# Kernel tuning notes

Hardware: AMD Instinct MI355X
Metric: run time of the kernel (lower is better)

The kernel has to match this reference:

```python
import jax, jax.numpy as jnp
import numpy as np

B, C, L = 8, 256, 2048


def setup_inputs() -> dict:
    key = jax.random.key(0)
    ks = jax.random.split(key, 7)
    s = 0.05
    return {
        "x": jax.random.normal(ks[0], (B, C, L), dtype=jnp.float32),
        "Wq": jax.random.normal(ks[1], (C, C), dtype=jnp.float32) * s,
        "bq": jax.random.normal(ks[2], (C,), dtype=jnp.float32) * s,
        "Wk": jax.random.normal(ks[3], (C, C), dtype=jnp.float32) * s,
        "bk": jax.random.normal(ks[4], (C,), dtype=jnp.float32) * s,
        "Wv": jax.random.normal(ks[5], (C, C), dtype=jnp.float32) * s,
        "bv": jax.random.normal(ks[6], (C,), dtype=jnp.float32) * s,
    }


def reference(x, Wq, bq, Wk, bk, Wv, bv):
    # Conv1d with kernel_size=1 == per-position linear over channels.
    # x: [B, C, L]
    scale = x.shape[1] ** (-0.5)
    q = jnp.einsum('oc,bcl->bol', Wq, x) + bq[None, :, None]  # [B,C,L]
    k = jnp.einsum('oc,bcl->bol', Wk, x) + bk[None, :, None]
    v = jnp.einsum('oc,bcl->bol', Wv, x) + bv[None, :, None]
    scores = jnp.einsum('bcl,bcm->blm', q, k) * scale          # [B,L,L]
    attn = jax.nn.softmax(scores, axis=-1)
    context = jnp.einsum('blm,bcm->bcl', attn, v)              # [B,C,L]
    return context + x
```

## Files before the change

### kernel.cpp

```cpp
#include <hip/hip_runtime.h>

#define NB 8
#define NC 256
#define NL 2048
#define SCALE 0.0625f

typedef __attribute__((ext_vector_type(8))) __bf16 bf16x8;
typedef __attribute__((ext_vector_type(4))) float f32x4;
typedef __attribute__((ext_vector_type(4))) unsigned int u32x4;
typedef __attribute__((ext_vector_type(2))) unsigned int u32x2;
typedef __attribute__((ext_vector_type(4))) unsigned short u16x4;
typedef __attribute__((ext_vector_type(8))) unsigned short u16x8;

static __device__ __forceinline__ unsigned short f2b(float f) {
    unsigned int u = __builtin_bit_cast(unsigned int, f);
    u += 0x7fffu + ((u >> 16) & 1u);
    return (unsigned short)(u >> 16);
}

__global__ void wconv_kernel(const float* __restrict__ Wq,
                             const float* __restrict__ Wk,
                             const float* __restrict__ Wv,
                             unsigned short* __restrict__ Wbf)
{
    const int base = (blockIdx.x * 256 + threadIdx.x) * 4;
    const int mat  = base >> 16;
    const int off  = base & 65535;
    const float* W = (mat == 0) ? Wq : (mat == 1) ? Wk : Wv;
    float4 w = *(const float4*)&W[off];
    u16x4 p = {f2b(w.x), f2b(w.y), f2b(w.z), f2b(w.w)};
    *(u16x4*)&Wbf[base] = p;
}

__global__ __launch_bounds__(256, 2) void xprep_kernel(
    const float* __restrict__ x, unsigned short* __restrict__ xT)
{
    const int b  = blockIdx.z;
    const int c0 = blockIdx.y * 64;
    const int l0 = blockIdx.x * 64;
    const int t  = threadIdx.x;

    __shared__ unsigned short Tr[64][68];

    #pragma unroll
    for (int p = 0; p < 4; ++p) {
        const int c  = p * 16 + (t >> 4);
        const int lg = t & 15;
        float4 xv = *(const float4*)&x[((size_t)(b * NC + c0 + c)) * NL + l0 + lg * 4];
        u16x4 pk = {f2b(xv.x), f2b(xv.y), f2b(xv.z), f2b(xv.w)};
        *(u16x4*)&Tr[c][lg * 4] = pk;
    }
    __syncthreads();
    #pragma unroll
    for (int j = 0; j < 2; ++j) {
        const int chunk = t + 256 * j;
        const int l  = chunk >> 3;
        const int ck = chunk & 7;
        u16x8 o;
        #pragma unroll
        for (int i = 0; i < 8; ++i) o[i] = Tr[ck * 8 + i][l];
        *(u16x8*)&xT[((size_t)(b * NL + l0 + l)) * NC + c0 + ck * 8] = o;
    }
}

__global__ __launch_bounds__(256, 2) void qkv_mfma(
    const unsigned short* __restrict__ xT,
    const unsigned short* __restrict__ Wbf,
    const float* __restrict__ bq, const float* __restrict__ bk,
    const float* __restrict__ bv,
    unsigned short* __restrict__ qT, unsigned short* __restrict__ kT,
    unsigned short* __restrict__ vo)
{
    const int raw = blockIdx.x;
    const int b   = raw & 7;
    const int rem = raw >> 3;
    const int mat = rem >> 5;
    const int lt0 = (rem & 31) * 64;
    const int t    = threadIdx.x;
    const int w    = t >> 6;
    const int lane = t & 63;
    const int ln15 = lane & 15;
    const int quad = lane >> 4;

    __shared__ __align__(16) unsigned short XT[64 * 256];
    __shared__ __align__(16) unsigned short WC[256 * 64];

    const unsigned short* Wm = Wbf + mat * 65536;
    const float* bias = (mat == 0) ? bq : (mat == 1) ? bk : bv;

    float bvals[4][4];
    #pragma unroll
    for (int ot = 0; ot < 4; ++ot)
        #pragma unroll
        for (int r = 0; r < 4; ++r)
            bvals[ot][r] = bias[w * 64 + ot * 16 + quad * 4 + r];

    #pragma unroll
    for (int s = 0; s < 8; ++s) {
        const int il = w * 8 + s;
        const int n  = il * 2 + (lane >> 5);
        const int p  = lane & 31;
        const int g  = p ^ (n & 15);
        const unsigned short* gp = &xT[((size_t)(b * NL + lt0 + n)) * NC + g * 8];
        __builtin_amdgcn_global_load_lds(
            (const __attribute__((address_space(1))) unsigned int*)gp,
            (__attribute__((address_space(3))) unsigned int*)&XT[il * 512],
            16, 0, 0);
    }

    f32x4 acc[4][4];
    #pragma unroll
    for (int i = 0; i < 4; ++i)
        #pragma unroll
        for (int j = 0; j < 4; ++j) acc[i][j] = f32x4{0.f, 0.f, 0.f, 0.f};

    for (int k0 = 0; k0 < 4; ++k0) {
        if (k0) __syncthreads();
        #pragma unroll
        for (int s = 0; s < 8; ++s) {
            const int il = w * 8 + s;
            const int o  = il * 8 + (lane >> 3);
            const int p  = lane & 7;
            const int g  = p ^ (o & 7);
            const unsigned short* gp = &Wm[(size_t)o * NC + k0 * 64 + g * 8];
            __builtin_amdgcn_global_load_lds(
                (const __attribute__((address_space(1))) unsigned int*)gp,
                (__attribute__((address_space(3))) unsigned int*)&WC[il * 512],
                16, 0, 0);
        }
        __syncthreads();

        #pragma unroll
        for (int ks = 0; ks < 2; ++ks) {
            bf16x8 xf[4];
            #pragma unroll
            for (int lt = 0; lt < 4; ++lt) {
                const int l  = lt * 16 + ln15;
                const int kc = k0 * 8 + ks * 4 + quad;
                const int pp = kc ^ (l & 15);
                xf[lt] = __builtin_bit_cast(bf16x8, *(const u32x4*)&XT[l * 256 + pp * 8]);
            }
            #pragma unroll
            for (int ot = 0; ot < 4; ++ot) {
                const int o  = w * 64 + ot * 16 + ln15;
                const int pp = (ks * 4 + quad) ^ (o & 7);
                bf16x8 wf = __builtin_bit_cast(bf16x8, *(const u32x4*)&WC[o * 64 + pp * 8]);
                #pragma unroll
                for (int lt = 0; lt < 4; ++lt)
                    acc[ot][lt] = __builtin_amdgcn_mfma_f32_16x16x32_bf16(
                                      wf, xf[lt], acc[ot][lt], 0, 0, 0);
            }
        }
    }

    if (mat < 2) {
        unsigned short* out = (mat == 0) ? qT : kT;
        #pragma unroll
        for (int ot = 0; ot < 4; ++ot) {
            const int o_base = w * 64 + ot * 16 + quad * 4;
            #pragma unroll
            for (int lt = 0; lt < 4; ++lt) {
                const int l = lt0 + lt * 16 + ln15;
                u16x4 pk;
                #pragma unroll
                for (int r = 0; r < 4; ++r)
                    pk[r] = f2b(acc[ot][lt][r] + bvals[ot][r]);
                *(u16x4*)&out[((size_t)(b * NL + l)) * NC + o_base] = pk;
            }
        }
    } else {
        #pragma unroll
        for (int ot = 0; ot < 4; ++ot)
            #pragma unroll
            for (int lt = 0; lt < 4; ++lt) {
                const int l = lt0 + lt * 16 + ln15;
                #pragma unroll
                for (int r = 0; r < 4; ++r) {
                    const int o = w * 64 + ot * 16 + quad * 4 + r;
                    vo[((size_t)(b * NC + o)) * NL + l] = f2b(acc[ot][lt][r] + bvals[ot][r]);
                }
            }
    }
}

__global__ __launch_bounds__(1024, 4) void attn_kernel(
    const unsigned short* __restrict__ qT,
    const unsigned short* __restrict__ kT,
    const unsigned short* __restrict__ v,
    const float* __restrict__ x,
    float* __restrict__ out)
{
    const int raw  = blockIdx.x;
    const int b    = raw & 7;
    const int l0   = (raw >> 3) * 64;
    const int t    = threadIdx.x;
    const int w    = t >> 6;
    const int lane = t & 63;
    const int ln15 = lane & 15;
    const int quad = lane >> 4;
    const int qg   = w & 3;
    const int kg   = w >> 2;

    __shared__ __align__(16) char smem[147456];
    unsigned short* Kb0 = (unsigned short*)smem;
    unsigned short* Vb0 = (unsigned short*)(smem + 32768);
    unsigned short* Kb1 = (unsigned short*)(smem + 65536);
    unsigned short* Vb1 = (unsigned short*)(smem + 98304);
    char* P0 = smem + 131072;
    char* P1 = smem + 139264;
    float (*buf)[68] = (float(*)[68])smem;

    bf16x8 qf[8];
    {
        const size_t qrow = ((size_t)b * NL + l0 + qg * 16 + ln15) * NC;
        #pragma unroll
        for (int kt = 0; kt < 8; ++kt)
            qf[kt] = __builtin_bit_cast(bf16x8,
                        *(const u32x4*)&qT[qrow + kt * 32 + quad * 8]);
    }

    f32x4 ctx[4];
    #pragma unroll
    for (int i = 0; i < 4; ++i) ctx[i] = f32x4{0.f, 0.f, 0.f, 0.f};
    f32x4 dacc = f32x4{0.f, 0.f, 0.f, 0.f};

    const u16x8 ones_u = {0x3F80, 0x3F80, 0x3F80, 0x3F80,
                          0x3F80, 0x3F80, 0x3F80, 0x3F80};
    const bf16x8 onesf = __builtin_bit_cast(bf16x8, ones_u);

    auto stageK = [&](int mt, unsigned short* Kd) {
        const int m0 = mt * 64;
        #pragma unroll
        for (int s = 0; s < 2; ++s) {
            const int il = w * 2 + s;
            const int n  = il * 2 + (lane >> 5);
            const int g  = (lane & 31) ^ (n & 15);
            const unsigned short* gp = &kT[((size_t)b * NL + m0 + n) * NC + g * 8];
            __builtin_amdgcn_global_load_lds(
                (const __attribute__((address_space(1))) unsigned int*)gp,
                (__attribute__((address_space(3))) unsigned int*)&Kd[il * 512],
                16, 0, 0);
        }
    };
    auto stageV = [&](int mt, unsigned short* Vd) {
        const int m0 = mt * 64;
        #pragma unroll
        for (int s = 0; s < 2; ++s) {
            const int il = w * 2 + s;
            const int c  = il * 8 + (lane >> 3);
            const int g  = (lane & 7) ^ (c & 7);
            const unsigned short* gp = &v[((size_t)(b * NC + c)) * NL + m0 + g * 8];
            __builtin_amdgcn_global_load_lds(
                (const __attribute__((address_space(1))) unsigned int*)gp,
                (__attribute__((address_space(3))) unsigned int*)&Vd[il * 512],
                16, 0, 0);
        }
    };

    const int q    = qg * 16 + ln15;
    const int pwof = q * 128 + (((kg * 32) + quad * 8) ^ ((q & 7) << 4));
    int prof[2];
    #pragma unroll
    for (int jw = 0; jw < 2; ++jw)
        prof[jw] = q * 128 + ((jw * 64 + quad * 16) ^ ((q & 7) << 4));

    stageK(0, Kb0);
    __syncthreads();

    for (int mt = 0; mt <= 32; ++mt) {
        if (mt < 31) stageK(mt + 1, (mt & 1) ? Kb0 : Kb1);
        if (mt < 32) stageV(mt, (mt & 1) ? Vb1 : Vb0);

        f32x4 sacc0 = f32x4{0.f, 0.f, 0.f, 0.f};
        f32x4 sacc1 = f32x4{0.f, 0.f, 0.f, 0.f};
        if (mt < 32) {
            const unsigned short* Kd = (mt & 1) ? Kb1 : Kb0;
            const int n = kg * 16 + ln15;
            #pragma unroll
            for (int kt = 0; kt < 8; kt += 2) {
                const int p0 = (kt * 4 + quad) ^ (n & 15);
                const int p1 = ((kt + 1) * 4 + quad) ^ (n & 15);
                bf16x8 kf0 = __builtin_bit_cast(bf16x8,
                               *(const u32x4*)&Kd[n * 256 + p0 * 8]);
                bf16x8 kf1 = __builtin_bit_cast(bf16x8,
                               *(const u32x4*)&Kd[n * 256 + p1 * 8]);
                sacc0 = __builtin_amdgcn_mfma_f32_16x16x32_bf16(
                            kf0, qf[kt], sacc0, 0, 0, 0);
                sacc1 = __builtin_amdgcn_mfma_f32_16x16x32_bf16(
                            kf1, qf[kt + 1], sacc1, 0, 0, 0);
            }
        }

        if (mt > 0) {
            const char* Pr = ((mt - 1) & 1) ? P1 : P0;
            const unsigned short* Vd = ((mt - 1) & 1) ? Vb1 : Vb0;
            bf16x8 pa[2];
            #pragma unroll
            for (int jw = 0; jw < 2; ++jw)
                pa[jw] = __builtin_bit_cast(bf16x8, *(const u32x4*)(Pr + prof[jw]));
            dacc = __builtin_amdgcn_mfma_f32_16x16x32_bf16(pa[0], onesf, dacc, 0, 0, 0);
            dacc = __builtin_amdgcn_mfma_f32_16x16x32_bf16(pa[1], onesf, dacc, 0, 0, 0);
            #pragma unroll
            for (int ct = 0; ct < 4; ++ct) {
                const int c = kg * 64 + ct * 16 + ln15;
                #pragma unroll
                for (int jw = 0; jw < 2; ++jw) {
                    const int p = (jw * 4 + quad) ^ (c & 7);
                    bf16x8 vb = __builtin_bit_cast(bf16x8,
                                  *(const u32x4*)&Vd[c * 64 + p * 8]);
                    ctx[ct] = __builtin_amdgcn_mfma_f32_16x16x32_bf16(
                                  pa[jw], vb, ctx[ct], 0, 0, 0);
                }
            }
        }

        if (mt < 32) {
            char* Pw = (mt & 1) ? P1 : P0;
            float e0 = __expf((sacc0[0] + sacc1[0]) * SCALE);
            float e1 = __expf((sacc0[1] + sacc1[1]) * SCALE);
            float e2 = __expf((sacc0[2] + sacc1[2]) * SCALE);
            float e3 = __expf((sacc0[3] + sacc1[3]) * SCALE);
            unsigned int d0 = (unsigned int)f2b(e0) | ((unsigned int)f2b(e1) << 16);
            unsigned int d1 = (unsigned int)f2b(e2) | ((unsigned int)f2b(e3) << 16);
            *(u32x2*)(Pw + pwof) = u32x2{d0, d1};
        }

        __syncthreads();
    }

    {
        float rinv[4];
        #pragma unroll
        for (int r = 0; r < 4; ++r) rinv[r] = 1.0f / dacc[r];
        #pragma unroll
        for (int ct = 0; ct < 4; ++ct) {
            const int c = kg * 64 + ct * 16 + ln15;
            #pragma unroll
            for (int r = 0; r < 4; ++r)
                buf[c][qg * 16 + quad * 4 + r] = ctx[ct][r] * rinv[r];
        }
    }
    __syncthreads();

    #pragma unroll
    for (int p = 0; p < 4; ++p) {
        const int f  = t + 1024 * p;
        const int c  = f >> 4;
        const int lg = (f & 15) * 4;
        const size_t idx = ((size_t)(b * NC + c)) * NL + l0 + lg;
        float4 xv = *(const float4*)&x[idx];
        float4 cv = *(const float4*)&buf[c][lg];
        float4 o = make_float4(cv.x + xv.x, cv.y + xv.y, cv.z + xv.z, cv.w + xv.w);
        *(float4*)&out[idx] = o;
    }
}

extern "C" void kernel_launch(void* const* d_in, const int* in_sizes, int n_in,
                              void* d_out, int out_size, void* d_ws, size_t ws_size,
                              hipStream_t stream) {
    const float* x  = (const float*)d_in[0];
    const float* Wq = (const float*)d_in[1];
    const float* bq = (const float*)d_in[2];
    const float* Wk = (const float*)d_in[3];
    const float* bk = (const float*)d_in[4];
    const float* Wv = (const float*)d_in[5];
    const float* bv = (const float*)d_in[6];
    float* out = (float*)d_out;

    const size_t plane = (size_t)NB * NC * NL;
    unsigned short* qT  = (unsigned short*)d_ws;
    unsigned short* kT  = qT + plane;
    unsigned short* v   = kT + plane;
    unsigned short* xT  = v + plane;
    unsigned short* Wbf = xT + plane;

    wconv_kernel<<<192, 256, 0, stream>>>(Wq, Wk, Wv, Wbf);

    dim3 gx(NL / 64, NC / 64, NB);
    xprep_kernel<<<gx, 256, 0, stream>>>(x, xT);

    qkv_mfma<<<768, 256, 0, stream>>>(xT, Wbf, bq, bk, bv, qT, kT, v);

    attn_kernel<<<256, 1024, 0, stream>>>(qT, kT, v, x, out);
}
```

Measured before the change: 153.6 us.

## Merge weight and x prep kernels; stage V output through LDS for coalesced stores

Folds the weight bf16 conversion into the x transpose/convert kernel as extra blocks, removing one kernel launch. In the QKV projection, the V output was written as scattered 2-byte stores along L. It now goes into a shared-memory tile first and is written back as 16-byte row-contiguous stores. This adds two barriers and reuses the XT/WC shared buffers for the staging tile.

```diff
diff --git a/kernel.cpp b/kernel.cpp
--- a/kernel.cpp
+++ b/kernel.cpp
@@ -18,29 +18,30 @@
     return (unsigned short)(u >> 16);
 }
 
-__global__ void wconv_kernel(const float* __restrict__ Wq,
-                             const float* __restrict__ Wk,
-                             const float* __restrict__ Wv,
-                             unsigned short* __restrict__ Wbf)
+__global__ __launch_bounds__(256) void prep_kernel(
+    const float* __restrict__ x, unsigned short* __restrict__ xT,
+    const float* __restrict__ Wq, const float* __restrict__ Wk,
+    const float* __restrict__ Wv, unsigned short* __restrict__ Wbf)
 {
-    const int base = (blockIdx.x * 256 + threadIdx.x) * 4;
-    const int mat  = base >> 16;
-    const int off  = base & 65535;
-    const float* W = (mat == 0) ? Wq : (mat == 1) ? Wk : Wv;
-    float4 w = *(const float4*)&W[off];
-    u16x4 p = {f2b(w.x), f2b(w.y), f2b(w.z), f2b(w.w)};
-    *(u16x4*)&Wbf[base] = p;
-}
-
-__global__ __launch_bounds__(256, 2) void xprep_kernel(
-    const float* __restrict__ x, unsigned short* __restrict__ xT)
-{
-    const int b  = blockIdx.z;
-    const int c0 = blockIdx.y * 64;
-    const int l0 = blockIdx.x * 64;
-    const int t  = threadIdx.x;
+    const int blk = blockIdx.x;
+    const int t   = threadIdx.x;
 
     __shared__ unsigned short Tr[64][68];
+
+    if (blk >= 1024) {
+        const int base = ((blk - 1024) * 256 + t) * 4;
+        const int mat  = base >> 16;
+        const int off  = base & 65535;
+        const float* W = (mat == 0) ? Wq : (mat == 1) ? Wk : Wv;
+        float4 w = *(const float4*)&W[off];
+        u16x4 p = {f2b(w.x), f2b(w.y), f2b(w.z), f2b(w.w)};
+        *(u16x4*)&Wbf[base] = p;
+        return;
+    }
+
+    const int b  = blk >> 7;
+    const int c0 = ((blk >> 5) & 3) * 64;
+    const int l0 = (blk & 31) * 64;
 
     #pragma unroll
     for (int p = 0; p < 4; ++p) {
@@ -82,8 +83,10 @@
     const int ln15 = lane & 15;
     const int quad = lane >> 4;
 
-    __shared__ __align__(16) unsigned short XT[64 * 256];
-    __shared__ __align__(16) unsigned short WC[256 * 64];
+    __shared__ __align__(16) char qsmem[65536];
+    unsigned short* XT = (unsigned short*)qsmem;
+    unsigned short* WC = (unsigned short*)(qsmem + 32768);
+    unsigned short (*Vst)[68] = (unsigned short(*)[68])qsmem;
 
     const unsigned short* Wm = Wbf + mat * 65536;
     const float* bias = (mat == 0) ? bq : (mat == 1) ? bk : bv;
@@ -169,17 +172,25 @@
             }
         }
     } else {
+        __syncthreads();
         #pragma unroll
         for (int ot = 0; ot < 4; ++ot)
             #pragma unroll
             for (int lt = 0; lt < 4; ++lt) {
-                const int l = lt0 + lt * 16 + ln15;
                 #pragma unroll
                 for (int r = 0; r < 4; ++r) {
                     const int o = w * 64 + ot * 16 + quad * 4 + r;
-                    vo[((size_t)(b * NC + o)) * NL + l] = f2b(acc[ot][lt][r] + bvals[ot][r]);
+                    Vst[o][lt * 16 + ln15] = f2b(acc[ot][lt][r] + bvals[ot][r]);
                 }
             }
+        __syncthreads();
+        #pragma unroll
+        for (int p = 0; p < 8; ++p) {
+            const int row = (t >> 3) + 32 * p;
+            const int col = (t & 7) * 8;
+            u16x8 val = *(const u16x8*)&Vst[row][col];
+            *(u16x8*)&vo[((size_t)(b * NC + row)) * NL + lt0 + col] = val;
+        }
     }
 }
 
@@ -374,10 +385,7 @@
     unsigned short* xT  = v + plane;
     unsigned short* Wbf = xT + plane;
 
-    wconv_kernel<<<192, 256, 0, stream>>>(Wq, Wk, Wv, Wbf);
-
-    dim3 gx(NL / 64, NC / 64, NB);
-    xprep_kernel<<<gx, 256, 0, stream>>>(x, xT);
+    prep_kernel<<<1216, 256, 0, stream>>>(x, xT, Wq, Wk, Wv, Wbf);
 
     qkv_mfma<<<768, 256, 0, stream>>>(xT, Wbf, bq, bk, bv, qT, kT, v);
 
```

Result: faster. 150.0 us (-2.4%).
